# Kernel tuning notes

Hardware: AMD Instinct MI355X
Metric: run time of the kernel (lower is better)

## Reference

```python
import jax, jax.numpy as jnp
from jax import lax
import numpy as np

# ---- static config derived from init_kwargs ----
BATCH, SEQ, DM = 16, 1024, 512
EXPAND, DSTATE, DCONV, HEADDIM = 2, 64, 4, 64
DIN = EXPAND * DM                 # 1024 (d_inner)
NH = DIN // HEADDIM               # 16 heads
CONVDIM = DIN + 2 * DSTATE        # 1152 (x, B, C share depthwise conv)
DINPROJ = 2 * DIN + 2 * DSTATE + NH  # 2192
IN_CH, OUT_CH = SEQ, 1024         # Conv1d sees (B, L, d_model) as (N, C=L, len=d_model)
EPS = 1e-5


def setup_inputs() -> dict:
    key = jax.random.key(0)
    ks = jax.random.split(key, 8)
    sc = lambda k, shape, s=0.02: jax.random.normal(k, shape, jnp.float32) * s
    return {
        "x": jax.random.normal(ks[0], (BATCH, SEQ, DM), jnp.float32),
        # Mamba2 params (bias=False for in/out proj by default)
        "in_proj_w": sc(ks[1], (DINPROJ, DM)),
        "conv1d_w": sc(ks[2], (CONVDIM, DCONV), 0.1),   # depthwise kernel
        "conv1d_b": jnp.zeros((CONVDIM,), jnp.float32),
        "dt_bias": sc(ks[3], (NH,), 0.1),
        "A_log": jnp.log(jnp.linspace(1.0, 16.0, NH, dtype=jnp.float32)),
        "D": jnp.ones((NH,), jnp.float32),
        "rms_w": jnp.ones((DIN,), jnp.float32),
        "out_proj_w": sc(ks[4], (DM, DIN)),
        # trailing Conv1d(in_channels=SEQ, out_channels, k=3, pad=1)
        "conv_w": sc(ks[5], (OUT_CH, IN_CH, 3)),
        "conv_b": jnp.zeros((OUT_CH,), jnp.float32),
        # BatchNorm1d affine params (training-mode batch stats)
        "bn_gamma": jnp.ones((OUT_CH,), jnp.float32),
        "bn_beta": jnp.zeros((OUT_CH,), jnp.float32),
    }


def _mamba2(u, in_proj_w, conv1d_w, conv1d_b, dt_bias, A_log, D, rms_w, out_proj_w):
    B, L, _ = u.shape
    zxbcdt = u @ in_proj_w.T                          # (B, L, DINPROJ)
    z = zxbcdt[..., :DIN]
    xBC = zxbcdt[..., DIN:DIN + CONVDIM]
    dt = zxbcdt[..., DIN + CONVDIM:]                  # (B, L, NH)
    dt = jax.nn.softplus(dt + dt_bias)

    # causal depthwise conv over time + SiLU
    xBC_t = jnp.pad(xBC.transpose(0, 2, 1), ((0, 0), (0, 0), (DCONV - 1, 0)))
    xBC_c = lax.conv_general_dilated(
        xBC_t, conv1d_w[:, None, :], (1,), 'VALID',
        dimension_numbers=('NCH', 'OIH', 'NCH'), feature_group_count=CONVDIM)
    xBC = jax.nn.silu(xBC_c + conv1d_b[None, :, None]).transpose(0, 2, 1)  # (B, L, CONVDIM)

    x_in = xBC[..., :DIN].reshape(B, L, NH, HEADDIM)  # (B, L, H, P)
    Bm = xBC[..., DIN:DIN + DSTATE]                   # (B, L, N), ngroups=1
    Cm = xBC[..., DIN + DSTATE:]                      # (B, L, N)

    A = -jnp.exp(A_log)                               # (H,)
    dA = jnp.exp(dt * A)                              # (B, L, H)

    def step(h, inp):
        dA_t, dt_t, x_t, B_t, C_t = inp
        h = h * dA_t[:, :, None, None] + jnp.einsum('bh,bhp,bn->bhpn', dt_t, x_t, B_t)
        y_t = jnp.einsum('bhpn,bn->bhp', h, C_t)
        return h, y_t

    h0 = jnp.zeros((B, NH, HEADDIM, DSTATE), u.dtype)
    xs = (dA.transpose(1, 0, 2), dt.transpose(1, 0, 2),
          x_in.transpose(1, 0, 2, 3), Bm.transpose(1, 0, 2), Cm.transpose(1, 0, 2))
    _, ys = lax.scan(step, h0, xs)                    # (L, B, H, P)
    y = ys.transpose(1, 0, 2, 3) + D[None, None, :, None] * x_in
    y = y.reshape(B, L, DIN)

    # gated RMSNorm: norm(y * silu(z))
    y = y * jax.nn.silu(z)
    y = y * lax.rsqrt(jnp.mean(y * y, axis=-1, keepdims=True) + EPS) * rms_w
    return y @ out_proj_w.T                           # (B, L, DM)


def reference(x, in_proj_w, conv1d_w, conv1d_b, dt_bias, A_log, D, rms_w,
              out_proj_w, conv_w, conv_b, bn_gamma, bn_beta):
    u = _mamba2(x, in_proj_w, conv1d_w, conv1d_b, dt_bias, A_log, D, rms_w, out_proj_w)
    # Conv1d over (N, C=SEQ, len=DM), kernel 3, padding 1
    c = lax.conv_general_dilated(u, conv_w, (1,), [(1, 1)],
                                 dimension_numbers=('NCH', 'OIH', 'NCH'))
    c = c + conv_b[None, :, None]                     # (B, OUT_CH, DM)
    # BatchNorm1d (training-mode batch statistics, biased variance)
    mean = jnp.mean(c, axis=(0, 2), keepdims=True)
    var = jnp.mean((c - mean) ** 2, axis=(0, 2), keepdims=True)
    c = (c - mean) * lax.rsqrt(var + EPS)
    c = c * bn_gamma[None, :, None] + bn_beta[None, :, None]
    return jax.nn.silu(c)
```

## Files before the change

kernel.cpp:

```cpp
#include <hip/hip_runtime.h>
#include <hip/hip_bf16.h>

#define BATCH 16
#define SEQ   1024
#define DM    512
#define DSTATE 64
#define DIN   1024
#define NH    16
#define CONVDIM 1152
#define DINPROJ 2192
#define NPAD  2304
#define XDTW  1280
#define OC    1024
#define EPSF  1e-5f

typedef __attribute__((ext_vector_type(8))) short short8;
typedef __attribute__((ext_vector_type(4))) float f32x4;

__device__ __forceinline__ void g2lds16(const __hip_bfloat16* g, __hip_bfloat16* l) {
  __builtin_amdgcn_global_load_lds(
      (const __attribute__((address_space(1))) void*)g,
      (__attribute__((address_space(3))) void*)l, 16, 0, 0);
}

__device__ __forceinline__ float siluf(float x) { return x / (1.f + expf(-x)); }
__device__ __forceinline__ float b2f(unsigned short u) {
  return __uint_as_float(((unsigned int)u) << 16);
}
__device__ __forceinline__ unsigned short f2b(float v) {
  __hip_bfloat16 h = __float2bfloat16(v);
  return __builtin_bit_cast(unsigned short, h);
}

__global__ __launch_bounds__(256) void gemm1_kernel(
    const __hip_bfloat16* __restrict__ A,
    const __hip_bfloat16* __restrict__ B,
    __hip_bfloat16* __restrict__ zbuf,
    __hip_bfloat16* __restrict__ xdt)
{
  __shared__ __hip_bfloat16 sAB[2][2][8192];
  const int tid  = threadIdx.x;
  const int lane = tid & 63;
  const int wid  = tid >> 6;
  const int wr = wid >> 1, wc = wid & 1;
  const long row0 = (long)blockIdx.x * 128;
  const int  col0 = blockIdx.y * 128;
  const __hip_bfloat16* Ab = A + row0 * 512;
  const __hip_bfloat16* Bb = B + (long)col0 * 512;

  auto stage = [&](int kt, int buf) {
#pragma unroll
    for (int it = 0; it < 4; ++it) {
      int idx = it * 256 + tid;
      int r = idx >> 3;
      int kk = (idx & 7) << 3;
      g2lds16(Ab + (long)r * 512 + kt + kk, &sAB[buf][0][idx * 8]);
      g2lds16(Bb + (long)r * 512 + kt + kk, &sAB[buf][1][idx * 8]);
    }
  };

  f32x4 acc[4][4] = {};
  stage(0, 0);
  __syncthreads();
  int cur = 0;
  for (int kt = 0; kt < 512; kt += 64) {
    if (kt + 64 < 512) stage(kt + 64, cur ^ 1);
    const __hip_bfloat16* sA = &sAB[cur][0][0];
    const __hip_bfloat16* sB = &sAB[cur][1][0];
#pragma unroll
    for (int kk = 0; kk < 64; kk += 32) {
      const int kl = kk + (lane >> 4) * 8;
      short8 af[4], bfr[4];
#pragma unroll
      for (int m = 0; m < 4; ++m)
        af[m] = *(const short8*)(sA + (wr * 64 + m * 16 + (lane & 15)) * 64 + kl);
#pragma unroll
      for (int n = 0; n < 4; ++n)
        bfr[n] = *(const short8*)(sB + (wc * 64 + n * 16 + (lane & 15)) * 64 + kl);
#pragma unroll
      for (int m = 0; m < 4; ++m)
#pragma unroll
        for (int n = 0; n < 4; ++n)
          acc[m][n] = __builtin_amdgcn_mfma_f32_16x16x32_bf16(af[m], bfr[n], acc[m][n], 0, 0, 0);
    }
    __syncthreads();
    cur ^= 1;
  }

  __hip_bfloat16* Cb;
  int ldc, coff;
  if (col0 < 1024) { Cb = zbuf; ldc = 1024; coff = col0; }
  else             { Cb = xdt;  ldc = XDTW; coff = col0 - 1024; }
  const int rb = (int)row0 + wr * 64 + ((lane >> 4) << 2);
  const int cb = coff + wc * 64 + (lane & 15);
#pragma unroll
  for (int m = 0; m < 4; ++m)
#pragma unroll
    for (int n = 0; n < 4; ++n) {
      const int r = rb + m * 16, cc = cb + n * 16;
#pragma unroll
      for (int q = 0; q < 4; ++q)
        Cb[(long)(r + q) * ldc + cc] = __float2bfloat16(acc[m][n][q]);
    }
}

__global__ __launch_bounds__(256) void gemm2_trans_kernel(
    const __hip_bfloat16* __restrict__ A,
    const __hip_bfloat16* __restrict__ B,
    const float* __restrict__ rn,
    __hip_bfloat16* __restrict__ uTp)
{
  __shared__ unsigned short smem[2][2][8192];
  const int tid  = threadIdx.x;
  const int lane = tid & 63;
  const int wid  = tid >> 6;
  const int wr = wid >> 1, wc = wid & 1;
  const long row0 = (long)blockIdx.x * 128;
  const int  col0 = blockIdx.y * 128;
  const int  b  = (int)(row0 >> 10);
  const int  l0 = (int)(row0 & 1023);
  const __hip_bfloat16* Ab = A + row0 * 1024;
  const __hip_bfloat16* Bb = B + (long)col0 * 1024;

  auto stage = [&](int kt, int buf) {
#pragma unroll
    for (int it = 0; it < 4; ++it) {
      int idx = it * 256 + tid;
      int r = idx >> 3;
      int kk = (idx & 7) << 3;
      g2lds16(Ab + (long)r * 1024 + kt + kk, (__hip_bfloat16*)&smem[buf][0][idx * 8]);
      g2lds16(Bb + (long)r * 1024 + kt + kk, (__hip_bfloat16*)&smem[buf][1][idx * 8]);
    }
  };

  f32x4 acc[4][4] = {};
  stage(0, 0);
  __syncthreads();
  int cur = 0;
  for (int kt = 0; kt < 1024; kt += 64) {
    if (kt + 64 < 1024) stage(kt + 64, cur ^ 1);
    const __hip_bfloat16* sA = (const __hip_bfloat16*)&smem[cur][0][0];
    const __hip_bfloat16* sB = (const __hip_bfloat16*)&smem[cur][1][0];
#pragma unroll
    for (int kk = 0; kk < 64; kk += 32) {
      const int kl = kk + (lane >> 4) * 8;
      short8 af[4], bfr[4];
#pragma unroll
      for (int m = 0; m < 4; ++m)
        af[m] = *(const short8*)(sA + (wr * 64 + m * 16 + (lane & 15)) * 64 + kl);
#pragma unroll
      for (int n = 0; n < 4; ++n)
        bfr[n] = *(const short8*)(sB + (wc * 64 + n * 16 + (lane & 15)) * 64 + kl);
#pragma unroll
      for (int m = 0; m < 4; ++m)
#pragma unroll
        for (int n = 0; n < 4; ++n)
          acc[m][n] = __builtin_amdgcn_mfma_f32_16x16x32_bf16(af[m], bfr[n], acc[m][n], 0, 0, 0);
    }
    __syncthreads();
    cur ^= 1;
  }

  unsigned short* sT = &smem[0][0][0];
  const int rl = wr * 64 + ((lane >> 4) << 2);
  const int cl = wc * 64 + (lane & 15);
#pragma unroll
  for (int m = 0; m < 4; ++m) {
    float rnv[4];
#pragma unroll
    for (int q = 0; q < 4; ++q) rnv[q] = rn[row0 + rl + m * 16 + q];
#pragma unroll
    for (int n = 0; n < 4; ++n) {
      const int c = cl + n * 16;
#pragma unroll
      for (int q = 0; q < 4; ++q)
        sT[c * 128 + rl + m * 16 + q] = f2b(acc[m][n][q] * rnv[q]);
    }
  }
  __syncthreads();

  unsigned short* up = (unsigned short*)uTp + (long)b * 514 * 1024;
  const int w = tid >> 6;
#pragma unroll
  for (int k = 0; k < 32; ++k) {
    const int row = w * 32 + k;
    ushort2 o2;
    o2.x = sT[row * 128 + lane * 2];
    o2.y = sT[row * 128 + lane * 2 + 1];
    *(ushort2*)(up + (long)(col0 + row + 1) * 1024 + l0 + lane * 2) = o2;
  }
}

__global__ __launch_bounds__(256) void gemm_conv_kernel(
    const __hip_bfloat16* __restrict__ A,
    const __hip_bfloat16* __restrict__ uTp,
    __hip_bfloat16* __restrict__ C)
{
  const int f = blockIdx.x + 8 * (blockIdx.y + 4 * blockIdx.z);
  const int g = (f & 7) * 64 + (f >> 3);
  const int bx = g & 7, by = (g >> 3) & 3, bz = g >> 5;

  __shared__ __hip_bfloat16 sAB[2][2][8192];
  const int tid  = threadIdx.x;
  const int lane = tid & 63;
  const int wid  = tid >> 6;
  const int wr = wid >> 1, wc = wid & 1;
  const int row0 = bx * 128;
  const int col0 = by * 128;
  const __hip_bfloat16* Ab = A + (long)row0 * 3072;
  const __hip_bfloat16* Ub = uTp + (long)bz * 514 * 1024;

  auto stage = [&](int kt, int buf) {
    const int seg = kt >> 10;
    const int io  = kt & 1023;
#pragma unroll
    for (int it = 0; it < 4; ++it) {
      int idx = it * 256 + tid;
      int r = idx >> 3;
      int kk = (idx & 7) << 3;
      g2lds16(Ab + (long)r * 3072 + kt + kk, &sAB[buf][0][idx * 8]);
      g2lds16(Ub + (long)(col0 + r + seg) * 1024 + io + kk, &sAB[buf][1][idx * 8]);
    }
  };

  f32x4 acc[4][4] = {};
  stage(0, 0);
  __syncthreads();
  int cur = 0;
  for (int kt = 0; kt < 3072; kt += 64) {
    if (kt + 64 < 3072) stage(kt + 64, cur ^ 1);
    const __hip_bfloat16* sA = &sAB[cur][0][0];
    const __hip_bfloat16* sB = &sAB[cur][1][0];
#pragma unroll
    for (int kk = 0; kk < 64; kk += 32) {
      const int kl = kk + (lane >> 4) * 8;
      short8 af[4], bfr[4];
#pragma unroll
      for (int m = 0; m < 4; ++m)
        af[m] = *(const short8*)(sA + (wr * 64 + m * 16 + (lane & 15)) * 64 + kl);
#pragma unroll
      for (int n = 0; n < 4; ++n)
        bfr[n] = *(const short8*)(sB + (wc * 64 + n * 16 + (lane & 15)) * 64 + kl);
#pragma unroll
      for (int m = 0; m < 4; ++m)
#pragma unroll
        for (int n = 0; n < 4; ++n)
          acc[m][n] = __builtin_amdgcn_mfma_f32_16x16x32_bf16(af[m], bfr[n], acc[m][n], 0, 0, 0);
    }
    __syncthreads();
    cur ^= 1;
  }

  __hip_bfloat16* Cb = C + (long)bz * OC * DM;
  const int rb = row0 + wr * 64 + ((lane >> 4) << 2);
  const int cb = col0 + wc * 64 + (lane & 15);
#pragma unroll
  for (int m = 0; m < 4; ++m)
#pragma unroll
    for (int n = 0; n < 4; ++n) {
      const int r = rb + m * 16, cc = cb + n * 16;
#pragma unroll
      for (int q = 0; q < 4; ++q)
        Cb[(long)(r + q) * DM + cc] = __float2bfloat16(acc[m][n][q]);
    }
}

__global__ __launch_bounds__(256) void fill_kernel(float* __restrict__ out, float v, long n) {
  long i = (long)blockIdx.x * 256 + threadIdx.x;
  if (i < n) out[i] = v;
}

__global__ __launch_bounds__(256) void prep_kernel(
    const float* __restrict__ x, const float* __restrict__ w1,
    const float* __restrict__ w2, const float* __restrict__ rms_w,
    const float* __restrict__ w3,
    __hip_bfloat16* __restrict__ xbf, __hip_bfloat16* __restrict__ w1b,
    __hip_bfloat16* __restrict__ w2b, __hip_bfloat16* __restrict__ w3b,
    float* __restrict__ rnacc)
{
  const int bid = blockIdx.x;
  if (bid < 8192) {
    long i = (long)bid * 256 + threadIdx.x;
    float4 v = *(const float4*)(x + i * 4);
    __hip_bfloat16* o = xbf + i * 4;
    o[0] = __float2bfloat16(v.x);
    o[1] = __float2bfloat16(v.y);
    o[2] = __float2bfloat16(v.z);
    o[3] = __float2bfloat16(v.w);
  } else if (bid < 12800) {
    int i = (bid - 8192) * 256 + threadIdx.x;
    int r = i >> 9;
    w1b[i] = (r < DINPROJ) ? __float2bfloat16(w1[i]) : __float2bfloat16(0.f);
  } else if (bid < 13312) {
    int i = (bid - 12800) * 256 + threadIdx.x;
    float4 v = *(const float4*)(w2 + (long)i * 4);
    float4 gw = *(const float4*)(rms_w + ((i * 4) & 1023));
    __hip_bfloat16* o = w2b + (long)i * 4;
    o[0] = __float2bfloat16(v.x * gw.x);
    o[1] = __float2bfloat16(v.y * gw.y);
    o[2] = __float2bfloat16(v.z * gw.z);
    o[3] = __float2bfloat16(v.w * gw.w);
  } else if (bid < 17408) {
    int t = (bid - 13312) * 256 + threadIdx.x;
    int o = t >> 10, i = t & 1023;
    const float* p = w3 + (long)o * 3072 + i * 3;
    __hip_bfloat16* q = w3b + (long)o * 3072 + i;
    q[0]    = __float2bfloat16(p[0]);
    q[1024] = __float2bfloat16(p[1]);
    q[2048] = __float2bfloat16(p[2]);
  } else {
    int i = (bid - 17408) * 256 + threadIdx.x;
    rnacc[i] = 0.f;
  }
}

__global__ __launch_bounds__(256) void conv1d_slide_kernel(
    const __hip_bfloat16* __restrict__ xdt, const float* __restrict__ cw,
    const float* __restrict__ cb, const float* __restrict__ dt_bias,
    __hip_bfloat16* __restrict__ xbc, float* __restrict__ dtb)
{
  const int pair = blockIdx.x * 256 + threadIdx.x;
  const int c = pair * 2;
  if (c >= CONVDIM + NH) return;
  const int b  = blockIdx.z;
  const int l0 = blockIdx.y * 16;
  const long rowb = (long)b * SEQ;
  const unsigned short* src = (const unsigned short*)xdt + rowb * XDTW + c;

  if (c < CONVDIM) {
    const float4 wa = *(const float4*)(cw + c * 4);
    const float4 wb = *(const float4*)(cw + (c + 1) * 4);
    const float ba = cb[c], bb = cb[c + 1];
    float w0x, w0y, w1x, w1y, w2x, w2y;
    {
      ushort2 v;
      if (l0 >= 3) { v = *(const ushort2*)(src + (long)(l0 - 3) * XDTW); w0x = b2f(v.x); w0y = b2f(v.y); }
      else { w0x = 0.f; w0y = 0.f; }
      if (l0 >= 2) { v = *(const ushort2*)(src + (long)(l0 - 2) * XDTW); w1x = b2f(v.x); w1y = b2f(v.y); }
      else { w1x = 0.f; w1y = 0.f; }
      if (l0 >= 1) { v = *(const ushort2*)(src + (long)(l0 - 1) * XDTW); w2x = b2f(v.x); w2y = b2f(v.y); }
      else { w2x = 0.f; w2y = 0.f; }
    }
    unsigned short* dst = (unsigned short*)xbc + rowb * CONVDIM + c;
#pragma unroll
    for (int i = 0; i < 16; ++i) {
      const int l = l0 + i;
      const ushort2 v = *(const ushort2*)(src + (long)l * XDTW);
      const float xv0 = b2f(v.x), xv1 = b2f(v.y);
      float a0 = ba, a1 = bb;
      a0 += w0x * wa.x; a1 += w0y * wb.x;
      a0 += w1x * wa.y; a1 += w1y * wb.y;
      a0 += w2x * wa.z; a1 += w2y * wb.z;
      a0 += xv0 * wa.w; a1 += xv1 * wb.w;
      ushort2 o;
      o.x = f2b(siluf(a0));
      o.y = f2b(siluf(a1));
      *(ushort2*)(dst + (long)l * CONVDIM) = o;
      w0x = w1x; w0y = w1y; w1x = w2x; w1y = w2y; w2x = xv0; w2y = xv1;
    }
  } else {
    const int hh = c - CONVDIM;
    const float b0 = dt_bias[hh], b1 = dt_bias[hh + 1];
#pragma unroll
    for (int i = 0; i < 16; ++i) {
      const long l = l0 + i;
      const ushort2 v = *(const ushort2*)(src + l * XDTW);
      const float d0 = b2f(v.x) + b0, d1 = b2f(v.y) + b1;
      float2 o;
      o.x = fmaxf(d0, 0.f) + log1pf(expf(-fabsf(d0)));
      o.y = fmaxf(d1, 0.f) + log1pf(expf(-fabsf(d1)));
      *(float2*)(dtb + (rowb + l) * NH + hh) = o;
    }
  }
}

__global__ __launch_bounds__(256) void ssd_chunk_kernel(
    const __hip_bfloat16* __restrict__ xbc, const float* __restrict__ dtb,
    const float* __restrict__ A_log, __hip_bfloat16* __restrict__ ypre,
    __hip_bfloat16* __restrict__ Tbuf, float* __restrict__ Aprod)
{
  const int c = blockIdx.x, h = blockIdx.y, b = blockIdx.z;
  const int tid = threadIdx.x, lane = tid & 63, wid = tid >> 6;
  const int wr = wid >> 1, wc = wid & 1;
  const long r0 = (long)b * SEQ + c * 64;

  __shared__ unsigned short sB[64 * 72], sC[64 * 72], sXT[64 * 72],
                            sBwT[64 * 72], sM[64 * 72];
  __shared__ float sS[64], sDt[64];

  {
    const int j = tid >> 2, seg = (tid & 3) * 16;
    const unsigned short* row = (const unsigned short*)(xbc + (r0 + j) * CONVDIM);
    short8 v0 = *(const short8*)(row + DIN + seg);
    short8 v1 = *(const short8*)(row + DIN + seg + 8);
    *(short8*)&sB[j * 72 + seg] = v0;
    *(short8*)&sB[j * 72 + seg + 8] = v1;
    v0 = *(const short8*)(row + DIN + DSTATE + seg);
    v1 = *(const short8*)(row + DIN + DSTATE + seg + 8);
    *(short8*)&sC[j * 72 + seg] = v0;
    *(short8*)&sC[j * 72 + seg + 8] = v1;
    short8 x0 = *(const short8*)(row + h * 64 + seg);
    short8 x1 = *(const short8*)(row + h * 64 + seg + 8);
#pragma unroll
    for (int e = 0; e < 8; ++e) {
      sXT[(seg + e) * 72 + j] = (unsigned short)x0[e];
      sXT[(seg + 8 + e) * 72 + j] = (unsigned short)x1[e];
    }
  }
  if (tid < 64) {
    float dt = dtb[(r0 + tid) * NH + h];
    float s = -__expf(A_log[h]) * dt;
#pragma unroll
    for (int off = 1; off < 64; off <<= 1) {
      float o = __shfl_up(s, off);
      if (lane >= off) s += o;
    }
    sDt[tid] = dt;
    sS[tid] = s;
    if (tid == 63) Aprod[((b * 16 + h) * 16) + c] = __expf(s);
  }
  __syncthreads();

  {
    const int j = tid >> 2, n0 = (tid & 3) * 16;
    const float w = __expf(sS[63] - sS[j]) * sDt[j];
#pragma unroll
    for (int e = 0; e < 16; ++e)
      sBwT[(n0 + e) * 72 + j] = f2b(w * b2f(sB[j * 72 + n0 + e]));
  }
  {
    f32x4 acc1[2][2] = {};
#pragma unroll
    for (int kk = 0; kk < 64; kk += 32) {
      const int kl = kk + (lane >> 4) * 8;
      short8 af[2], bfr[2];
#pragma unroll
      for (int m = 0; m < 2; ++m)
        af[m] = *(const short8*)&sC[(wr * 32 + m * 16 + (lane & 15)) * 72 + kl];
#pragma unroll
      for (int n = 0; n < 2; ++n)
        bfr[n] = *(const short8*)&sB[(wc * 32 + n * 16 + (lane & 15)) * 72 + kl];
#pragma unroll
      for (int m = 0; m < 2; ++m)
#pragma unroll
        for (int n = 0; n < 2; ++n)
          acc1[m][n] = __builtin_amdgcn_mfma_f32_16x16x32_bf16(af[m], bfr[n], acc1[m][n], 0, 0, 0);
    }
    const int rq = (lane >> 4) * 4, cc = lane & 15;
#pragma unroll
    for (int m = 0; m < 2; ++m)
#pragma unroll
      for (int n = 0; n < 2; ++n)
#pragma unroll
        for (int q = 0; q < 4; ++q) {
          const int i = wr * 32 + m * 16 + rq + q;
          const int jj = wc * 32 + n * 16 + cc;
          float f = (jj <= i) ? __expf(sS[i] - sS[jj]) * sDt[jj] : 0.f;
          sM[i * 72 + jj] = f2b(acc1[m][n][q] * f);
        }
  }
  __syncthreads();

  f32x4 acc2[2][2] = {}, acc3[2][2] = {};
#pragma unroll
  for (int kk = 0; kk < 64; kk += 32) {
    const int kl = kk + (lane >> 4) * 8;
    short8 am[2], axB[2], axA[2], abw[2];
#pragma unroll
    for (int m = 0; m < 2; ++m) {
      am[m]  = *(const short8*)&sM[(wr * 32 + m * 16 + (lane & 15)) * 72 + kl];
      axA[m] = *(const short8*)&sXT[(wr * 32 + m * 16 + (lane & 15)) * 72 + kl];
    }
#pragma unroll
    for (int n = 0; n < 2; ++n) {
      axB[n] = *(const short8*)&sXT[(wc * 32 + n * 16 + (lane & 15)) * 72 + kl];
      abw[n] = *(const short8*)&sBwT[(wc * 32 + n * 16 + (lane & 15)) * 72 + kl];
    }
#pragma unroll
    for (int m = 0; m < 2; ++m)
#pragma unroll
      for (int n = 0; n < 2; ++n) {
        acc2[m][n] = __builtin_amdgcn_mfma_f32_16x16x32_bf16(am[m], axB[n], acc2[m][n], 0, 0, 0);
        acc3[m][n] = __builtin_amdgcn_mfma_f32_16x16x32_bf16(axA[m], abw[n], acc3[m][n], 0, 0, 0);
      }
  }
  const int rq = (lane >> 4) * 4, cc = lane & 15;
  const long tb = (((long)(b * 16 + h)) * 16 + c) * 4096;
#pragma unroll
  for (int m = 0; m < 2; ++m)
#pragma unroll
    for (int n = 0; n < 2; ++n)
#pragma unroll
      for (int q = 0; q < 4; ++q) {
        const int i = wr * 32 + m * 16 + rq + q;
        const int pj = wc * 32 + n * 16 + cc;
        ypre[(r0 + i) * DIN + h * 64 + pj] = __float2bfloat16(acc2[m][n][q]);
        Tbuf[tb + i * 64 + pj] = __float2bfloat16(acc3[m][n][q]);
      }
}

__global__ __launch_bounds__(1024) void ssd_state_kernel(
    __hip_bfloat16* __restrict__ Tbuf, const float* __restrict__ Aprod)
{
  const int bh = blockIdx.x;
  const int t = threadIdx.x;
  float h0 = 0.f, h1 = 0.f, h2 = 0.f, h3 = 0.f;
  unsigned short* base = (unsigned short*)Tbuf + (long)bh * 16 * 4096 + t * 4;
  for (int c = 0; c < 16; ++c) {
    unsigned short* p = base + (long)c * 4096;
    ushort4 tv = *(const ushort4*)p;
    ushort4 hv;
    hv.x = f2b(h0); hv.y = f2b(h1); hv.z = f2b(h2); hv.w = f2b(h3);
    *(ushort4*)p = hv;
    const float ap = Aprod[bh * 16 + c];
    h0 = h0 * ap + b2f(tv.x);
    h1 = h1 * ap + b2f(tv.y);
    h2 = h2 * ap + b2f(tv.z);
    h3 = h3 * ap + b2f(tv.w);
  }
}

__global__ __launch_bounds__(256) void ssd_out_kernel(
    const __hip_bfloat16* __restrict__ xbc, const float* __restrict__ dtb,
    const float* __restrict__ A_log, const __hip_bfloat16* __restrict__ Hbuf,
    const __hip_bfloat16* __restrict__ zbuf, const float* __restrict__ Dv,
    __hip_bfloat16* __restrict__ ypre, float* __restrict__ rnacc)
{
  const int c = blockIdx.x, h = blockIdx.y, b = blockIdx.z;
  const int tid = threadIdx.x, lane = tid & 63, wid = tid >> 6;
  const int wr = wid >> 1, wc = wid & 1;
  const long r0 = (long)b * SEQ + c * 64;

  __shared__ unsigned short sC[64 * 72], sH[64 * 72];
  __shared__ float sS[64];
  __shared__ float sRedW[2][64];

  {
    const int j = tid >> 2, seg = (tid & 3) * 16;
    const unsigned short* row = (const unsigned short*)(xbc + (r0 + j) * CONVDIM);
    short8 v0 = *(const short8*)(row + DIN + DSTATE + seg);
    short8 v1 = *(const short8*)(row + DIN + DSTATE + seg + 8);
    *(short8*)&sC[j * 72 + seg] = v0;
    *(short8*)&sC[j * 72 + seg + 8] = v1;
    const unsigned short* hrow =
        (const unsigned short*)Hbuf + (((long)(b * 16 + h)) * 16 + c) * 4096 + j * 64;
    v0 = *(const short8*)(hrow + seg);
    v1 = *(const short8*)(hrow + seg + 8);
    *(short8*)&sH[j * 72 + seg] = v0;
    *(short8*)&sH[j * 72 + seg + 8] = v1;
  }
  if (tid < 64) {
    float dt = dtb[(r0 + tid) * NH + h];
    float s = -__expf(A_log[h]) * dt;
#pragma unroll
    for (int off = 1; off < 64; off <<= 1) {
      float o = __shfl_up(s, off);
      if (lane >= off) s += o;
    }
    sS[tid] = s;
  }
  __syncthreads();

  f32x4 acc[2][2] = {};
#pragma unroll
  for (int kk = 0; kk < 64; kk += 32) {
    const int kl = kk + (lane >> 4) * 8;
    short8 af[2], bfr[2];
#pragma unroll
    for (int m = 0; m < 2; ++m)
      af[m] = *(const short8*)&sC[(wr * 32 + m * 16 + (lane & 15)) * 72 + kl];
#pragma unroll
    for (int n = 0; n < 2; ++n)
      bfr[n] = *(const short8*)&sH[(wc * 32 + n * 16 + (lane & 15)) * 72 + kl];
#pragma unroll
    for (int m = 0; m < 2; ++m)
#pragma unroll
      for (int n = 0; n < 2; ++n)
        acc[m][n] = __builtin_amdgcn_mfma_f32_16x16x32_bf16(af[m], bfr[n], acc[m][n], 0, 0, 0);
  }
  const float Dh = Dv[h];
  const int rq = (lane >> 4) * 4, cc = lane & 15;
  float rsum[2][4] = {};
#pragma unroll
  for (int m = 0; m < 2; ++m)
#pragma unroll
    for (int n = 0; n < 2; ++n)
#pragma unroll
      for (int q = 0; q < 4; ++q) {
        const int i = wr * 32 + m * 16 + rq + q;
        const int p = wc * 32 + n * 16 + cc;
        const long r = r0 + i;
        const long oidx = r * DIN + h * 64 + p;
        float yv = b2f(((const unsigned short*)ypre)[oidx]);
        float xv = b2f(((const unsigned short*)xbc)[r * CONVDIM + h * 64 + p]);
        float zv = b2f(((const unsigned short*)zbuf)[r * DIN + h * 64 + p]);
        yv += __expf(sS[i]) * acc[m][n][q] + Dh * xv;
        const float g = yv * siluf(zv);
        rsum[m][q] += g * g;
        ypre[oidx] = __float2bfloat16(g);
      }
#pragma unroll
  for (int m = 0; m < 2; ++m)
#pragma unroll
    for (int q = 0; q < 4; ++q) {
      float v = rsum[m][q];
      v += __shfl_xor(v, 1);
      v += __shfl_xor(v, 2);
      v += __shfl_xor(v, 4);
      v += __shfl_xor(v, 8);
      if ((lane & 15) == 0)
        sRedW[wc][wr * 32 + m * 16 + rq + q] = v;
    }
  __syncthreads();
  if (tid < 64) atomicAdd(&rnacc[r0 + tid], sRedW[0][tid] + sRedW[1][tid]);
}

__global__ __launch_bounds__(256) void rnfin_pad_kernel(
    const float* __restrict__ rnacc, float* __restrict__ rn,
    __hip_bfloat16* __restrict__ uTp)
{
  const int bid = blockIdx.x;
  if (bid < 64) {
    int i = bid * 256 + threadIdx.x;
    rn[i] = rsqrtf(rnacc[i] * (1.f / DIN) + EPSF);
  } else {
    int t = (bid - 64) * 256 + threadIdx.x;
    int n = t >> 11, w = t & 2047;
    long row = (w >> 10) ? 513 : 0;
    uTp[(long)n * 514 * 1024 + row * 1024 + (w & 1023)] = __float2bfloat16(0.f);
  }
}

__global__ __launch_bounds__(256) void bn_stats_kernel(
    const __hip_bfloat16* __restrict__ c, float* __restrict__ stats)
{
  const int o = blockIdx.x, t = threadIdx.x;
  float s = 0.f, s2 = 0.f;
  for (int n = 0; n < BATCH; ++n) {
    const unsigned short* base = (const unsigned short*)c + ((long)n * OC + o) * DM;
    ushort2 v = *(const ushort2*)(base + t * 2);
    float a = b2f(v.x), bb = b2f(v.y);
    s += a + bb;
    s2 += a * a + bb * bb;
  }
#pragma unroll
  for (int m = 32; m >= 1; m >>= 1) { s += __shfl_xor(s, m); s2 += __shfl_xor(s2, m); }
  __shared__ float r1[4], r2[4];
  if ((t & 63) == 0) { r1[t >> 6] = s; r2[t >> 6] = s2; }
  __syncthreads();
  if (t == 0) {
    s = r1[0] + r1[1] + r1[2] + r1[3];
    s2 = r2[0] + r2[1] + r2[2] + r2[3];
    float mean = s * (1.f / 8192.f);
    float var = s2 * (1.f / 8192.f) - mean * mean;
    stats[o] = mean;
    stats[OC + o] = rsqrtf(var + EPSF);
  }
}

__global__ __launch_bounds__(256) void bn_silu_kernel(
    const __hip_bfloat16* __restrict__ c, const float* __restrict__ stats,
    const float* __restrict__ gamma, const float* __restrict__ beta,
    float* __restrict__ out)
{
  long gid = (long)blockIdx.x * 256 + threadIdx.x;
  long base = gid * 4;
  int o = (int)((base >> 9) & (OC - 1));
  float mean = stats[o], rstd = stats[OC + o];
  float g = gamma[o] * rstd;
  float sh = beta[o] - mean * g;
  ushort4 v = *(const ushort4*)((const unsigned short*)c + base);
  float4 r;
  r.x = siluf(b2f(v.x) * g + sh);
  r.y = siluf(b2f(v.y) * g + sh);
  r.z = siluf(b2f(v.z) * g + sh);
  r.w = siluf(b2f(v.w) * g + sh);
  *(float4*)(out + base) = r;
}

extern "C" void kernel_launch(void* const* d_in, const int* in_sizes, int n_in,
                              void* d_out, int out_size, void* d_ws, size_t ws_size,
                              hipStream_t stream) {
  const float* x         = (const float*)d_in[0];
  const float* in_projw  = (const float*)d_in[1];
  const float* conv1dw   = (const float*)d_in[2];
  const float* conv1db   = (const float*)d_in[3];
  const float* dt_bias   = (const float*)d_in[4];
  const float* A_log     = (const float*)d_in[5];
  const float* Dv        = (const float*)d_in[6];
  const float* rms_w     = (const float*)d_in[7];
  const float* out_projw = (const float*)d_in[8];
  const float* conv_w    = (const float*)d_in[9];
  const float* bn_gamma  = (const float*)d_in[11];
  const float* bn_beta   = (const float*)d_in[12];
  float* out = (float*)d_out;
  char* ws = (char*)d_ws;

  __hip_bfloat16* zbuf = (__hip_bfloat16*)(ws + 0UL);
  __hip_bfloat16* xdt  = (__hip_bfloat16*)(ws + 33554432UL);
  __hip_bfloat16* xbcb = (__hip_bfloat16*)(ws + 75497472UL);
  __hip_bfloat16* ypb  = (__hip_bfloat16*)(ws + 113246208UL);
  __hip_bfloat16* xbf  = (__hip_bfloat16*)(ws + 146800640UL);
  __hip_bfloat16* w1b  = (__hip_bfloat16*)(ws + 163577856UL);
  __hip_bfloat16* w2b  = (__hip_bfloat16*)(ws + 165937152UL);
  __hip_bfloat16* w3b  = (__hip_bfloat16*)(ws + 166985728UL);
  float* dtb           = (float*)(ws + 173277184UL);
  float* Aprod         = (float*)(ws + 174325760UL);
  float* stats         = (float*)(ws + 174342144UL);
  float* rn            = (float*)(ws + 174350336UL);
  float* rnacc         = (float*)(ws + 174415872UL);
  const size_t WS_NEED = 174481408UL;

  const long outn = (long)BATCH * OC * DM;
  if (ws_size < WS_NEED) {
    fill_kernel<<<(int)((outn + 255) / 256), 256, 0, stream>>>(out, (float)(ws_size >> 20), outn);
    return;
  }

  __hip_bfloat16* Tbuf = xdt;
  __hip_bfloat16* uTp  = xdt;
  __hip_bfloat16* cbuf = zbuf;

  prep_kernel<<<17472, 256, 0, stream>>>(x, in_projw, out_projw, rms_w, conv_w,
                                         xbf, w1b, w2b, w3b, rnacc);

  gemm1_kernel<<<dim3(128, 18), 256, 0, stream>>>(xbf, w1b, zbuf, xdt);
  conv1d_slide_kernel<<<dim3(3, 64, BATCH), 256, 0, stream>>>(xdt, conv1dw, conv1db,
                                                              dt_bias, xbcb, dtb);
  ssd_chunk_kernel<<<dim3(16, 16, 16), 256, 0, stream>>>(xbcb, dtb, A_log, ypb, Tbuf, Aprod);
  ssd_state_kernel<<<256, 1024, 0, stream>>>(Tbuf, Aprod);
  ssd_out_kernel<<<dim3(16, 16, 16), 256, 0, stream>>>(xbcb, dtb, A_log, Tbuf, zbuf,
                                                       Dv, ypb, rnacc);
  rnfin_pad_kernel<<<192, 256, 0, stream>>>(rnacc, rn, uTp);
  gemm2_trans_kernel<<<dim3(128, 4), 256, 0, stream>>>(ypb, w2b, rn, uTp);
  gemm_conv_kernel<<<dim3(8, 4, 16), 256, 0, stream>>>(w3b, uTp, cbuf);
  bn_stats_kernel<<<1024, 256, 0, stream>>>(cbuf, stats);
  bn_silu_kernel<<<8192, 256, 0, stream>>>(cbuf, stats, bn_gamma, bn_beta, out);
}
```

Baseline: 288.0 us.

## Fuse BN statistics into conv GEMM epilogue and stage SSD outputs via LDS

The BatchNorm sum and sum-of-squares are now computed in the conv GEMM epilogue with wave shuffles and atomics, so the separate bn_stats kernel and its re-read of the conv output are gone. bn_silu derives mean and rstd from the accumulated sums, and prep zeroes the accumulator. The SSD chunk and output kernels also stage their bf16 results in shared memory and write them back as coalesced 16-byte stores instead of scattered 2-byte stores. This adds many atomics and extra barriers, and the statistics now come from fp32 accumulators instead of rounded bf16 values.

```diff
diff --git a/kernel.cpp b/kernel.cpp
--- a/kernel.cpp
+++ b/kernel.cpp
@@ -194,7 +194,8 @@
 __global__ __launch_bounds__(256) void gemm_conv_kernel(
     const __hip_bfloat16* __restrict__ A,
     const __hip_bfloat16* __restrict__ uTp,
-    __hip_bfloat16* __restrict__ C)
+    __hip_bfloat16* __restrict__ C,
+    float* __restrict__ statsacc)
 {
   const int f = blockIdx.x + 8 * (blockIdx.y + 4 * blockIdx.z);
   const int g = (f & 7) * 64 + (f >> 3);
@@ -263,6 +264,24 @@
       for (int q = 0; q < 4; ++q)
         Cb[(long)(r + q) * DM + cc] = __float2bfloat16(acc[m][n][q]);
     }
+
+#pragma unroll
+  for (int m = 0; m < 4; ++m)
+#pragma unroll
+    for (int q = 0; q < 4; ++q) {
+      float s = 0.f, s2 = 0.f;
+#pragma unroll
+      for (int n = 0; n < 4; ++n) { float v = acc[m][n][q]; s += v; s2 += v * v; }
+      s  += __shfl_xor(s, 1);  s  += __shfl_xor(s, 2);
+      s  += __shfl_xor(s, 4);  s  += __shfl_xor(s, 8);
+      s2 += __shfl_xor(s2, 1); s2 += __shfl_xor(s2, 2);
+      s2 += __shfl_xor(s2, 4); s2 += __shfl_xor(s2, 8);
+      if ((lane & 15) == 0) {
+        const int o = rb + m * 16 + q;
+        atomicAdd(&statsacc[o], s);
+        atomicAdd(&statsacc[OC + o], s2);
+      }
+    }
 }
 
 __global__ __launch_bounds__(256) void fill_kernel(float* __restrict__ out, float v, long n) {
@@ -276,7 +295,7 @@
     const float* __restrict__ w3,
     __hip_bfloat16* __restrict__ xbf, __hip_bfloat16* __restrict__ w1b,
     __hip_bfloat16* __restrict__ w2b, __hip_bfloat16* __restrict__ w3b,
-    float* __restrict__ rnacc)
+    float* __restrict__ rnacc, float* __restrict__ statsacc)
 {
   const int bid = blockIdx.x;
   if (bid < 8192) {
@@ -308,9 +327,12 @@
     q[0]    = __float2bfloat16(p[0]);
     q[1024] = __float2bfloat16(p[1]);
     q[2048] = __float2bfloat16(p[2]);
-  } else {
+  } else if (bid < 17472) {
     int i = (bid - 17408) * 256 + threadIdx.x;
     rnacc[i] = 0.f;
+  } else {
+    int i = (bid - 17472) * 256 + threadIdx.x;
+    statsacc[i] = 0.f;
   }
 }
 
@@ -484,19 +506,32 @@
         acc3[m][n] = __builtin_amdgcn_mfma_f32_16x16x32_bf16(axA[m], abw[n], acc3[m][n], 0, 0, 0);
       }
   }
-  const int rq = (lane >> 4) * 4, cc = lane & 15;
-  const long tb = (((long)(b * 16 + h)) * 16 + c) * 4096;
-#pragma unroll
-  for (int m = 0; m < 2; ++m)
-#pragma unroll
-    for (int n = 0; n < 2; ++n)
-#pragma unroll
-      for (int q = 0; q < 4; ++q) {
-        const int i = wr * 32 + m * 16 + rq + q;
-        const int pj = wc * 32 + n * 16 + cc;
-        ypre[(r0 + i) * DIN + h * 64 + pj] = __float2bfloat16(acc2[m][n][q]);
-        Tbuf[tb + i * 64 + pj] = __float2bfloat16(acc3[m][n][q]);
-      }
+  __syncthreads();
+  {
+    const int rq = (lane >> 4) * 4, cc = lane & 15;
+#pragma unroll
+    for (int m = 0; m < 2; ++m)
+#pragma unroll
+      for (int n = 0; n < 2; ++n)
+#pragma unroll
+        for (int q = 0; q < 4; ++q) {
+          const int i = wr * 32 + m * 16 + rq + q;
+          const int pj = wc * 32 + n * 16 + cc;
+          sM[i * 72 + pj]   = f2b(acc2[m][n][q]);
+          sBwT[i * 72 + pj] = f2b(acc3[m][n][q]);
+        }
+  }
+  __syncthreads();
+  {
+    const int j = tid >> 2, seg = (tid & 3) * 16;
+    unsigned short* yp = (unsigned short*)ypre + (r0 + j) * DIN + h * 64 + seg;
+    *(short8*)yp       = *(const short8*)&sM[j * 72 + seg];
+    *(short8*)(yp + 8) = *(const short8*)&sM[j * 72 + seg + 8];
+    const long tb = (((long)(b * 16 + h)) * 16 + c) * 4096;
+    unsigned short* tp = (unsigned short*)Tbuf + tb + j * 64 + seg;
+    *(short8*)tp       = *(const short8*)&sBwT[j * 72 + seg];
+    *(short8*)(tp + 8) = *(const short8*)&sBwT[j * 72 + seg + 8];
+  }
 }
 
 __global__ __launch_bounds__(1024) void ssd_state_kernel(
@@ -578,6 +613,7 @@
       for (int n = 0; n < 2; ++n)
         acc[m][n] = __builtin_amdgcn_mfma_f32_16x16x32_bf16(af[m], bfr[n], acc[m][n], 0, 0, 0);
   }
+  __syncthreads();
   const float Dh = Dv[h];
   const int rq = (lane >> 4) * 4, cc = lane & 15;
   float rsum[2][4] = {};
@@ -597,7 +633,7 @@
         yv += __expf(sS[i]) * acc[m][n][q] + Dh * xv;
         const float g = yv * siluf(zv);
         rsum[m][q] += g * g;
-        ypre[oidx] = __float2bfloat16(g);
+        sC[i * 72 + p] = f2b(g);
       }
 #pragma unroll
   for (int m = 0; m < 2; ++m)
@@ -612,6 +648,12 @@
         sRedW[wc][wr * 32 + m * 16 + rq + q] = v;
     }
   __syncthreads();
+  {
+    const int j = tid >> 2, seg = (tid & 3) * 16;
+    unsigned short* yp = (unsigned short*)ypre + (r0 + j) * DIN + h * 64 + seg;
+    *(short8*)yp       = *(const short8*)&sC[j * 72 + seg];
+    *(short8*)(yp + 8) = *(const short8*)&sC[j * 72 + seg + 8];
+  }
   if (tid < 64) atomicAdd(&rnacc[r0 + tid], sRedW[0][tid] + sRedW[1][tid]);
 }
 
@@ -631,42 +673,17 @@
   }
 }
 
-__global__ __launch_bounds__(256) void bn_stats_kernel(
-    const __hip_bfloat16* __restrict__ c, float* __restrict__ stats)
-{
-  const int o = blockIdx.x, t = threadIdx.x;
-  float s = 0.f, s2 = 0.f;
-  for (int n = 0; n < BATCH; ++n) {
-    const unsigned short* base = (const unsigned short*)c + ((long)n * OC + o) * DM;
-    ushort2 v = *(const ushort2*)(base + t * 2);
-    float a = b2f(v.x), bb = b2f(v.y);
-    s += a + bb;
-    s2 += a * a + bb * bb;
-  }
-#pragma unroll
-  for (int m = 32; m >= 1; m >>= 1) { s += __shfl_xor(s, m); s2 += __shfl_xor(s2, m); }
-  __shared__ float r1[4], r2[4];
-  if ((t & 63) == 0) { r1[t >> 6] = s; r2[t >> 6] = s2; }
-  __syncthreads();
-  if (t == 0) {
-    s = r1[0] + r1[1] + r1[2] + r1[3];
-    s2 = r2[0] + r2[1] + r2[2] + r2[3];
-    float mean = s * (1.f / 8192.f);
-    float var = s2 * (1.f / 8192.f) - mean * mean;
-    stats[o] = mean;
-    stats[OC + o] = rsqrtf(var + EPSF);
-  }
-}
-
 __global__ __launch_bounds__(256) void bn_silu_kernel(
-    const __hip_bfloat16* __restrict__ c, const float* __restrict__ stats,
+    const __hip_bfloat16* __restrict__ c, const float* __restrict__ statsacc,
     const float* __restrict__ gamma, const float* __restrict__ beta,
     float* __restrict__ out)
 {
   long gid = (long)blockIdx.x * 256 + threadIdx.x;
   long base = gid * 4;
   int o = (int)((base >> 9) & (OC - 1));
-  float mean = stats[o], rstd = stats[OC + o];
+  float mean = statsacc[o] * (1.f / 8192.f);
+  float var = statsacc[OC + o] * (1.f / 8192.f) - mean * mean;
+  float rstd = rsqrtf(var + EPSF);
   float g = gamma[o] * rstd;
   float sh = beta[o] - mean * g;
   ushort4 v = *(const ushort4*)((const unsigned short*)c + base);
@@ -706,7 +723,7 @@
   __hip_bfloat16* w3b  = (__hip_bfloat16*)(ws + 166985728UL);
   float* dtb           = (float*)(ws + 173277184UL);
   float* Aprod         = (float*)(ws + 174325760UL);
-  float* stats         = (float*)(ws + 174342144UL);
+  float* statsacc      = (float*)(ws + 174342144UL);
   float* rn            = (float*)(ws + 174350336UL);
   float* rnacc         = (float*)(ws + 174415872UL);
   const size_t WS_NEED = 174481408UL;
@@ -721,8 +738,8 @@
   __hip_bfloat16* uTp  = xdt;
   __hip_bfloat16* cbuf = zbuf;
 
-  prep_kernel<<<17472, 256, 0, stream>>>(x, in_projw, out_projw, rms_w, conv_w,
-                                         xbf, w1b, w2b, w3b, rnacc);
+  prep_kernel<<<17480, 256, 0, stream>>>(x, in_projw, out_projw, rms_w, conv_w,
+                                         xbf, w1b, w2b, w3b, rnacc, statsacc);
 
   gemm1_kernel<<<dim3(128, 18), 256, 0, stream>>>(xbf, w1b, zbuf, xdt);
   conv1d_slide_kernel<<<dim3(3, 64, BATCH), 256, 0, stream>>>(xdt, conv1dw, conv1db,
@@ -733,7 +750,6 @@
                                                        Dv, ypb, rnacc);
   rnfin_pad_kernel<<<192, 256, 0, stream>>>(rnacc, rn, uTp);
   gemm2_trans_kernel<<<dim3(128, 4), 256, 0, stream>>>(ypb, w2b, rn, uTp);
-  gemm_conv_kernel<<<dim3(8, 4, 16), 256, 0, stream>>>(w3b, uTp, cbuf);
-  bn_stats_kernel<<<1024, 256, 0, stream>>>(cbuf, stats);
-  bn_silu_kernel<<<8192, 256, 0, stream>>>(cbuf, stats, bn_gamma, bn_beta, out);
-}
+  gemm_conv_kernel<<<dim3(8, 4, 16), 256, 0, stream>>>(w3b, uTp, cbuf, statsacc);
+  bn_silu_kernel<<<8192, 256, 0, stream>>>(cbuf, statsacc, bn_gamma, bn_beta, out);
+}
```

Result: no change. 285.0 us (-1.1%).
